# Kernel optimization log

Hardware: AMD Instinct MI355X
Metric: run time of the kernel (lower is better)

Reference implementation:

```python
import jax, jax.numpy as jnp
import numpy as np

B, C, IMG, P, G = 512, 3, 128, 16, 8
DIM, HEADS, DH, DEPTH, MLP, NCLS, K = 384, 6, 64, 12, 1536, 1000, 16
N = G * G + 1  # 65 tokens (cls + 8x8 patches)
INNER = HEADS * DH
PD = C * P * P  # patch_dim = 768


def _rel_pos_index(g):
    coords = np.stack(np.meshgrid(np.arange(g), np.arange(g), indexing='ij')).reshape(2, -1)
    rel = (coords[:, :, None] - coords[:, None, :]).transpose(1, 2, 0)
    rel[..., 0] += g - 1
    rel[..., 1] += g - 1
    rel[..., 0] *= 2 * g - 1
    return jnp.asarray(rel.sum(-1))  # [g*g, g*g] int

REL_IDX = _rel_pos_index(G)


def _ln(x, w, b, eps=1e-5):
    mu = jnp.mean(x, -1, keepdims=True)
    var = jnp.mean((x - mu) ** 2, -1, keepdims=True)
    return (x - mu) * jax.lax.rsqrt(var + eps) * w + b


def setup_inputs() -> dict:
    key = jax.random.key(0)
    ks = iter(jax.random.split(key, 48))
    nrm = lambda shape, s=0.02: jax.random.normal(next(ks), shape, jnp.float32) * s
    return {
        'img': jax.random.normal(next(ks), (B, C, IMG, IMG), jnp.float32),
        'pe_ln1_w': jnp.ones((PD,), jnp.float32), 'pe_ln1_b': jnp.zeros((PD,), jnp.float32),
        'pe_w': nrm((PD, DIM)), 'pe_b': jnp.zeros((DIM,), jnp.float32),
        'pe_ln2_w': jnp.ones((DIM,), jnp.float32), 'pe_ln2_b': jnp.zeros((DIM,), jnp.float32),
        'cls_token': nrm((1, DIM), 1.0), 'pos_emb': nrm((N, DIM), 1.0),
        'attn_ln_w': jnp.ones((DEPTH, DIM), jnp.float32), 'attn_ln_b': jnp.zeros((DEPTH, DIM), jnp.float32),
        'qkv_w': nrm((DEPTH, DIM, 3 * INNER)),
        'out_w': nrm((DEPTH, INNER, DIM)), 'out_b': jnp.zeros((DEPTH, DIM), jnp.float32),
        'bias_tables': nrm((DEPTH, (2 * G - 1) * (2 * G - 1))),
        'ff_ln_w': jnp.ones((DEPTH, DIM), jnp.float32), 'ff_ln_b': jnp.zeros((DEPTH, DIM), jnp.float32),
        'ff_w1': nrm((DEPTH, DIM, MLP)), 'ff_b1': jnp.zeros((DEPTH, MLP), jnp.float32),
        'ff_w2': nrm((DEPTH, MLP, DIM)), 'ff_b2': jnp.zeros((DEPTH, DIM), jnp.float32),
        'final_ln_w': jnp.ones((DIM,), jnp.float32), 'final_ln_b': jnp.zeros((DIM,), jnp.float32),
        'head_w': nrm((DIM, NCLS)), 'head_b': jnp.zeros((NCLS,), jnp.float32),
    }


def reference(img, pe_ln1_w, pe_ln1_b, pe_w, pe_b, pe_ln2_w, pe_ln2_b, cls_token, pos_emb,
              attn_ln_w, attn_ln_b, qkv_w, out_w, out_b, bias_tables,
              ff_ln_w, ff_ln_b, ff_w1, ff_b1, ff_w2, ff_b2,
              final_ln_w, final_ln_b, head_w, head_b):
    b = img.shape[0]
    gh = IMG // P
    # b c (h p1) (w p2) -> b (h w) (p1 p2 c)
    x = img.reshape(b, C, gh, P, gh, P).transpose(0, 2, 4, 3, 5, 1).reshape(b, gh * gh, P * P * C)
    x = _ln(x, pe_ln1_w, pe_ln1_b)
    x = _ln(x @ pe_w + pe_b, pe_ln2_w, pe_ln2_b)
    cls = jnp.broadcast_to(cls_token[None], (b, 1, DIM))
    x = jnp.concatenate([cls, x], axis=1) + pos_emb[:N]
    scale = DH ** -0.5
    neg = jnp.finfo(jnp.float32).min  # == -finfo.max, matching torch masked_fill
    for i in range(DEPTH):
        h = _ln(x, attn_ln_w[i], attn_ln_b[i])
        qkv = h @ qkv_w[i]  # [b, N, 3*INNER]
        q, k, v = jnp.split(qkv, 3, axis=-1)
        q, k, v = [t.reshape(b, N, HEADS, DH).transpose(0, 2, 1, 3) for t in (q, k, v)]
        dots = jnp.einsum('bhid,bhjd->bhij', q, k) * scale
        full_bias = jnp.zeros((N, N), jnp.float32).at[1:, 1:].set(bias_tables[i][REL_IDX])
        dots = dots + full_bias
        _, idx = jax.lax.top_k(dots, K)  # per-query top-k keys
        mask = jnp.put_along_axis(jnp.zeros(dots.shape, bool), idx, True, axis=-1, inplace=False)
        attn = jax.nn.softmax(jnp.where(mask, dots, neg), axis=-1)
        o = jnp.einsum('bhij,bhjd->bhid', attn, v).transpose(0, 2, 1, 3).reshape(b, N, INNER)
        x = o @ out_w[i] + out_b[i] + x
        h = _ln(x, ff_ln_w[i], ff_ln_b[i])
        h = jax.nn.gelu(h @ ff_w1[i] + ff_b1[i], approximate=False)
        x = h @ ff_w2[i] + ff_b2[i] + x
    x = _ln(x, final_ln_w, final_ln_b)
    return x[:, 0] @ head_w + head_b
```

## Files before the change

kernel.cpp:

```cpp
#include <hip/hip_runtime.h>
#include <cstdint>
#include <cstddef>


typedef __attribute__((ext_vector_type(8))) short bf16x8;
typedef __attribute__((ext_vector_type(4))) float f32x4;
typedef __attribute__((ext_vector_type(4))) unsigned short u16x4;

__device__ __forceinline__ unsigned short f2bf(float f) {
  unsigned u = __float_as_uint(f);
  u += 0x7FFF + ((u >> 16) & 1);
  return (unsigned short)(u >> 16);
}
__device__ __forceinline__ float bf2f(unsigned short h) {
  return __uint_as_float(((unsigned)h) << 16);
}
__device__ __forceinline__ float gelu_f(float v) {
  return 0.5f * v * (1.f + erff(v * 0.70710678118654752440f));
}

typedef const __attribute__((address_space(1))) unsigned int* gas1_t;
typedef __attribute__((address_space(3))) unsigned int* las3_t;
__device__ __forceinline__ void async16(const void* g, void* l) {
  __builtin_amdgcn_global_load_lds((gas1_t)g, (las3_t)l, 16, 0, 0);
}

__global__ void k_tconv(const float* __restrict__ in, unsigned short* __restrict__ out,
                        int K, int N, int Npad, int total) {
  int idx = blockIdx.x * 256 + threadIdx.x;
  if (idx >= total) return;
  int per = Npad * K;
  int mat = idx / per;
  int rem = idx - mat * per;
  int n = rem / K;
  int kk = rem - n * K;
  float v = 0.f;
  if (n < N) v = in[(size_t)mat * K * N + (size_t)kk * N + n];
  out[idx] = f2bf(v);
}

__global__ void k_padhb(const float* __restrict__ hb, float* __restrict__ out) {
  int i = blockIdx.x * 256 + threadIdx.x;
  if (i < 1024) out[i] = (i < 1000) ? hb[i] : 0.f;
}

__global__ void k_patchln(const float* __restrict__ img,
                          const float* __restrict__ w1, const float* __restrict__ b1,
                          unsigned short* __restrict__ Xp) {
  const int p = blockIdx.x;
  const int b = p >> 6, pl = p & 63;
  const int gr = pl >> 3, gc = pl & 7;
  const int t = threadIdx.x;
  __shared__ float buf[768];
  __shared__ float ps[4], ps2[4];
#pragma unroll
  for (int s = 0; s < 3; ++s) {
    int rr = s * 16 + (t >> 4);
    int c = rr >> 4, p1 = rr & 15, p2 = t & 15;
    float v = img[(((size_t)b * 3 + c) * 128 + (gr * 16 + p1)) * 128 + gc * 16 + p2];
    buf[(p1 * 16 + p2) * 3 + c] = v;
  }
  __syncthreads();
  float e0 = buf[t], e1 = buf[t + 256], e2 = buf[t + 512];
  float s = e0 + e1 + e2;
  float s2 = e0 * e0 + e1 * e1 + e2 * e2;
  for (int off = 32; off; off >>= 1) { s += __shfl_xor(s, off); s2 += __shfl_xor(s2, off); }
  if ((t & 63) == 0) { ps[t >> 6] = s; ps2[t >> 6] = s2; }
  __syncthreads();
  float S = ps[0] + ps[1] + ps[2] + ps[3];
  float S2 = ps2[0] + ps2[1] + ps2[2] + ps2[3];
  float mu = S * (1.f / 768.f);
  float rs = rsqrtf(S2 * (1.f / 768.f) - mu * mu + 1e-5f);
  size_t ob = (size_t)p * 768;
  Xp[ob + t]       = f2bf((e0 - mu) * rs * w1[t]       + b1[t]);
  Xp[ob + t + 256] = f2bf((e1 - mu) * rs * w1[t + 256] + b1[t + 256]);
  Xp[ob + t + 512] = f2bf((e2 - mu) * rs * w1[t + 512] + b1[t + 512]);
}

__global__ void k_ln384(const float* __restrict__ X, const float* __restrict__ w,
                        const float* __restrict__ bb, unsigned short* __restrict__ H) {
  const int row = blockIdx.x;
  const int t = threadIdx.x;
  const float* xr = X + (size_t)row * 384;
  float e0 = xr[t], e1 = xr[t + 128], e2 = xr[t + 256];
  float s = e0 + e1 + e2, s2 = e0 * e0 + e1 * e1 + e2 * e2;
  for (int off = 32; off; off >>= 1) { s += __shfl_xor(s, off); s2 += __shfl_xor(s2, off); }
  __shared__ float ps[2], ps2[2];
  if ((t & 63) == 0) { ps[t >> 6] = s; ps2[t >> 6] = s2; }
  __syncthreads();
  float S = ps[0] + ps[1], S2 = ps2[0] + ps2[1];
  float mu = S * (1.f / 384.f);
  float rs = rsqrtf(S2 * (1.f / 384.f) - mu * mu + 1e-5f);
  size_t ob = (size_t)row * 384;
  H[ob + t]       = f2bf((e0 - mu) * rs * w[t]       + bb[t]);
  H[ob + t + 128] = f2bf((e1 - mu) * rs * w[t + 128] + bb[t + 128]);
  H[ob + t + 256] = f2bf((e2 - mu) * rs * w[t + 256] + bb[t + 256]);
}

__global__ void k_lncls(const float* __restrict__ X, const float* __restrict__ w,
                        const float* __restrict__ bb, unsigned short* __restrict__ H) {
  const int b = blockIdx.x;
  const int t = threadIdx.x;
  const float* xr = X + (size_t)b * 65 * 384;
  float e0 = xr[t], e1 = xr[t + 128], e2 = xr[t + 256];
  float s = e0 + e1 + e2, s2 = e0 * e0 + e1 * e1 + e2 * e2;
  for (int off = 32; off; off >>= 1) { s += __shfl_xor(s, off); s2 += __shfl_xor(s2, off); }
  __shared__ float ps[2], ps2[2];
  if ((t & 63) == 0) { ps[t >> 6] = s; ps2[t >> 6] = s2; }
  __syncthreads();
  float S = ps[0] + ps[1], S2 = ps2[0] + ps2[1];
  float mu = S * (1.f / 384.f);
  float rs = rsqrtf(S2 * (1.f / 384.f) - mu * mu + 1e-5f);
  size_t ob = (size_t)b * 384;
  H[ob + t]       = f2bf((e0 - mu) * rs * w[t]       + bb[t]);
  H[ob + t + 128] = f2bf((e1 - mu) * rs * w[t + 128] + bb[t + 128]);
  H[ob + t + 256] = f2bf((e2 - mu) * rs * w[t + 256] + bb[t + 256]);
}

__global__ void k_ln2pos(const float* __restrict__ tmp, const float* __restrict__ w,
                         const float* __restrict__ bb, const float* __restrict__ pos,
                         float* __restrict__ Xout) {
  const int p = blockIdx.x;
  const int b = p >> 6, pl = p & 63;
  const int t = threadIdx.x;
  const float* xr = tmp + (size_t)p * 384;
  float e0 = xr[t], e1 = xr[t + 128], e2 = xr[t + 256];
  float s = e0 + e1 + e2, s2 = e0 * e0 + e1 * e1 + e2 * e2;
  for (int off = 32; off; off >>= 1) { s += __shfl_xor(s, off); s2 += __shfl_xor(s2, off); }
  __shared__ float ps[2], ps2[2];
  if ((t & 63) == 0) { ps[t >> 6] = s; ps2[t >> 6] = s2; }
  __syncthreads();
  float S = ps[0] + ps[1], S2 = ps2[0] + ps2[1];
  float mu = S * (1.f / 384.f);
  float rs = rsqrtf(S2 * (1.f / 384.f) - mu * mu + 1e-5f);
  const float* pr = pos + (size_t)(1 + pl) * 384;
  float* orow = Xout + ((size_t)b * 65 + 1 + pl) * 384;
  orow[t]       = (e0 - mu) * rs * w[t]       + bb[t]       + pr[t];
  orow[t + 128] = (e1 - mu) * rs * w[t + 128] + bb[t + 128] + pr[t + 128];
  orow[t + 256] = (e2 - mu) * rs * w[t + 256] + bb[t + 256] + pr[t + 256];
}

__global__ void k_cls(const float* __restrict__ cls, const float* __restrict__ pos,
                      float* __restrict__ Xout) {
  int idx = blockIdx.x * 256 + threadIdx.x;
  if (idx >= 512 * 384) return;
  int b = idx / 384, d = idx - b * 384;
  Xout[(size_t)b * 65 * 384 + d] = cls[d] + pos[d];
}

template <int EPI, int OUTBF>
__global__ __launch_bounds__(256, 2) void k_gemm(
    const unsigned short* __restrict__ A,
    const unsigned short* __restrict__ Wt,
    const float* __restrict__ bias,
    const float* __restrict__ Res,
    void* __restrict__ Out,
    int K, int Nreal) {
  __shared__ alignas(16) unsigned short As[128 * 64];
  __shared__ alignas(16) unsigned short Bs[128 * 64];
  const int t = threadIdx.x;
  const int w = t >> 6, l = t & 63;
  const int m0 = blockIdx.x * 128, n0 = blockIdx.y * 128;
  const int wm = w & 1, wn = w >> 1;

  f32x4 acc[4][4] = {};

  const int rA = t >> 3;
  const int cb = t & 7;
  const unsigned short* Ag = A + (size_t)(m0 + rA) * K + cb * 8;
  const unsigned short* Bg = Wt + (size_t)(n0 + rA) * K + cb * 8;

  for (int k0 = 0; k0 < K; k0 += 64) {
#pragma unroll
    for (int p = 0; p < 4; ++p) {
      async16(Ag + (size_t)(p * 32) * K + k0, &As[p * 2048 + t * 8]);
      async16(Bg + (size_t)(p * 32) * K + k0, &Bs[p * 2048 + t * 8]);
    }
    __syncthreads();
#pragma unroll
    for (int kk = 0; kk < 64; kk += 32) {
      bf16x8 af[4], bfr[4];
      const int kof = kk + (l >> 4) * 8;
      const int rsel = l & 15;
#pragma unroll
      for (int i = 0; i < 4; ++i) {
        af[i]  = *(const bf16x8*)&As[(wm * 64 + i * 16 + rsel) * 64 + kof];
        bfr[i] = *(const bf16x8*)&Bs[(wn * 64 + i * 16 + rsel) * 64 + kof];
      }
#pragma unroll
      for (int i = 0; i < 4; ++i)
#pragma unroll
        for (int j = 0; j < 4; ++j)
          acc[i][j] = __builtin_amdgcn_mfma_f32_16x16x32_bf16(af[i], bfr[j], acc[i][j], 0, 0, 0);
    }
    __syncthreads();
  }

  const int colq = l & 15, rowq = (l >> 4) * 4;
#pragma unroll
  for (int i = 0; i < 4; ++i) {
    const int rb = m0 + wm * 64 + i * 16 + rowq;
#pragma unroll
    for (int j = 0; j < 4; ++j) {
      const int c = n0 + wn * 64 + j * 16 + colq;
      float bv = 0.f;
      if (EPI >= 1) bv = bias[c];
#pragma unroll
      for (int rg = 0; rg < 4; ++rg) {
        const int r = rb + rg;
        float v = acc[i][j][rg] + bv;
        if (EPI == 2) v = gelu_f(v);
        if (EPI == 3) v += Res[(size_t)r * Nreal + c];
        if (c < Nreal) {
          if (OUTBF) ((unsigned short*)Out)[(size_t)r * Nreal + c] = f2bf(v);
          else       ((float*)Out)[(size_t)r * Nreal + c] = v;
        }
      }
    }
  }
}

__global__ __launch_bounds__(256, 4) void k_attn(
    const unsigned short* __restrict__ qkvb,
    const float* __restrict__ btab,
    unsigned short* __restrict__ Obuf) {
  const int blk = blockIdx.x;
  const int b = blk / 6, h = blk - b * 6;
  __shared__ alignas(16) union UU {
    unsigned short qk[2 * 80 * 64];
    float ds[65 * 67];
  } u;
  __shared__ alignas(16) unsigned short vsb[65 * 64];
  __shared__ float wsel[65 * 16];
  __shared__ short seli[65 * 16];
  __shared__ float btl[225];
  const int t = threadIdx.x;
  const size_t base = (size_t)b * 65 * 1152 + h * 64;

  if (t < 225) btl[t] = btab[t];
  for (int idx = t; idx < 520; idx += 256) {
    int r = idx >> 3, c = idx & 7;
    const unsigned short* gp = qkvb + base + (size_t)r * 1152 + c * 8;
    async16(gp, &u.qk[idx * 8]);
    async16(gp + 384, &u.qk[80 * 64 + idx * 8]);
    async16(gp + 768, &vsb[idx * 8]);
  }
  __syncthreads();

  const int w = t >> 6, l = t & 63;
  f32x4 accs[7];
#pragma unroll
  for (int s = 0; s < 7; ++s) {
    int tt = w + s * 4;
    f32x4 a = {0.f, 0.f, 0.f, 0.f};
    if (tt < 25) {
      int it = tt / 5, jt = tt - it * 5;
#pragma unroll
      for (int kk = 0; kk < 64; kk += 32) {
        int kof = kk + (l >> 4) * 8;
        bf16x8 qa = *(const bf16x8*)&u.qk[(it * 16 + (l & 15)) * 64 + kof];
        bf16x8 kb = *(const bf16x8*)&u.qk[80 * 64 + (jt * 16 + (l & 15)) * 64 + kof];
        a = __builtin_amdgcn_mfma_f32_16x16x32_bf16(qa, kb, a, 0, 0, 0);
      }
    }
    accs[s] = a;
  }
  __syncthreads();

#pragma unroll
  for (int s = 0; s < 7; ++s) {
    int tt = w + s * 4;
    if (tt < 25) {
      int it = tt / 5, jt = tt - it * 5;
      int j = jt * 16 + (l & 15);
      int ib = it * 16 + (l >> 4) * 4;
      if (j < 65) {
#pragma unroll
        for (int rg = 0; rg < 4; ++rg) {
          int i = ib + rg;
          if (i < 65) {
            float bias = 0.f;
            if (i > 0 && j > 0) {
              int ri = (i - 1) >> 3, ci = (i - 1) & 7;
              int rj = (j - 1) >> 3, cj = (j - 1) & 7;
              bias = btl[(ri - rj + 7) * 15 + (ci - cj + 7)];
            }
            u.ds[i * 67 + j] = accs[s][rg] * 0.125f + bias;
          }
        }
      }
    }
  }
  __syncthreads();

  if (t < 65) {
    const float* dr = &u.ds[t * 67];
    float lv[16];
#pragma unroll
    for (int i = 0; i < 16; ++i) lv[i] = -3.4e38f;
    for (int j = 0; j < 65; ++j) {
      float x = dr[j];
#pragma unroll
      for (int i = 0; i < 16; ++i) {
        float lo = fminf(lv[i], x);
        lv[i] = fmaxf(lv[i], x);
        x = lo;
      }
    }
    float m0 = lv[0];
    float sum = 0.f;
#pragma unroll
    for (int i = 0; i < 16; ++i) sum += __expf(lv[i] - m0);
    float inv = 1.f / sum;
    float vt = lv[15];
    int pos = 0;
    for (int j = 0; j < 65; ++j) {
      float v = dr[j];
      if (v > vt) {
        wsel[t * 16 + pos] = v;
        seli[t * 16 + pos] = (short)j;
        ++pos;
      }
    }
    for (int j = 0; j < 65; ++j) {
      if (pos >= 16) break;
      float v = dr[j];
      if (v == vt) {
        wsel[t * 16 + pos] = v;
        seli[t * 16 + pos] = (short)j;
        ++pos;
      }
    }
#pragma unroll
    for (int i = 0; i < 16; ++i)
      wsel[t * 16 + i] = __expf(wsel[t * 16 + i] - m0) * inv;
  }
  __syncthreads();

  const size_t obase = (size_t)b * 65 * 384 + h * 64;
  for (int task = t; task < 65 * 16; task += 256) {
    int i = task >> 4, dc = task & 15;
    float a0 = 0.f, a1 = 0.f, a2 = 0.f, a3 = 0.f;
#pragma unroll
    for (int s = 0; s < 16; ++s) {
      float wv = wsel[i * 16 + s];
      int j = seli[i * 16 + s];
      u16x4 raw = *(const u16x4*)&vsb[j * 64 + dc * 4];
      a0 += wv * bf2f(raw.x);
      a1 += wv * bf2f(raw.y);
      a2 += wv * bf2f(raw.z);
      a3 += wv * bf2f(raw.w);
    }
    u16x4 o = {f2bf(a0), f2bf(a1), f2bf(a2), f2bf(a3)};
    *(u16x4*)&Obuf[obase + (size_t)i * 384 + dc * 4] = o;
  }
}

extern "C" void kernel_launch(void* const* d_in, const int* in_sizes, int n_in,
                              void* d_out, int out_size, void* d_ws, size_t ws_size,
                              hipStream_t stream) {
  (void)in_sizes; (void)n_in; (void)out_size; (void)ws_size;
  const float* img       = (const float*)d_in[0];
  const float* pe_ln1_w  = (const float*)d_in[1];
  const float* pe_ln1_b  = (const float*)d_in[2];
  const float* pe_w      = (const float*)d_in[3];
  const float* pe_b      = (const float*)d_in[4];
  const float* pe_ln2_w  = (const float*)d_in[5];
  const float* pe_ln2_b  = (const float*)d_in[6];
  const float* cls_tok   = (const float*)d_in[7];
  const float* pos_emb   = (const float*)d_in[8];
  const float* attn_ln_w = (const float*)d_in[9];
  const float* attn_ln_b = (const float*)d_in[10];
  const float* qkv_w     = (const float*)d_in[11];
  const float* out_w     = (const float*)d_in[12];
  const float* out_b     = (const float*)d_in[13];
  const float* btab      = (const float*)d_in[14];
  const float* ff_ln_w   = (const float*)d_in[15];
  const float* ff_ln_b   = (const float*)d_in[16];
  const float* ff_w1     = (const float*)d_in[17];
  const float* ff_b1     = (const float*)d_in[18];
  const float* ff_w2     = (const float*)d_in[19];
  const float* ff_b2     = (const float*)d_in[20];
  const float* fin_ln_w  = (const float*)d_in[21];
  const float* fin_ln_b  = (const float*)d_in[22];
  const float* head_w    = (const float*)d_in[23];
  const float* head_b    = (const float*)d_in[24];

  char* ws = (char*)d_ws;
  unsigned short* wt_pe   = (unsigned short*)(ws + 0);
  unsigned short* wt_qkv  = (unsigned short*)(ws + 589824);
  unsigned short* wt_out  = (unsigned short*)(ws + 11206656);
  unsigned short* wt_ff1  = (unsigned short*)(ws + 14745600);
  unsigned short* wt_ff2  = (unsigned short*)(ws + 28901376);
  unsigned short* wt_head = (unsigned short*)(ws + 43057152);
  float*          hb_pad  = (float*)(ws + 43843584);
  float*          x       = (float*)(ws + 43847680);
  unsigned short* hbuf    = (unsigned short*)(ws + 94965760);
  unsigned short* qkvb    = (unsigned short*)(ws + 120524800);
  unsigned short* h1      = (unsigned short*)(ws + 197201920);
  unsigned short* xcls    = (unsigned short*)(ws + 299438080);

  unsigned short* Xp = qkvb;
  float* tmp = (float*)h1;

  k_tconv<<<dim3((294912 + 255) / 256), 256, 0, stream>>>(pe_w, wt_pe, 768, 384, 384, 294912);
  k_tconv<<<dim3((5308416 + 255) / 256), 256, 0, stream>>>(qkv_w, wt_qkv, 384, 1152, 1152, 5308416);
  k_tconv<<<dim3((1769472 + 255) / 256), 256, 0, stream>>>(out_w, wt_out, 384, 384, 384, 1769472);
  k_tconv<<<dim3((7077888 + 255) / 256), 256, 0, stream>>>(ff_w1, wt_ff1, 384, 1536, 1536, 7077888);
  k_tconv<<<dim3((7077888 + 255) / 256), 256, 0, stream>>>(ff_w2, wt_ff2, 1536, 384, 384, 7077888);
  k_tconv<<<dim3((393216 + 255) / 256), 256, 0, stream>>>(head_w, wt_head, 384, 1000, 1024, 393216);
  k_padhb<<<4, 256, 0, stream>>>(head_b, hb_pad);

  k_patchln<<<32768, 256, 0, stream>>>(img, pe_ln1_w, pe_ln1_b, Xp);
  k_gemm<1, 0><<<dim3(256, 3), 256, 0, stream>>>(Xp, wt_pe, pe_b, nullptr, tmp, 768, 384);
  k_ln2pos<<<32768, 128, 0, stream>>>(tmp, pe_ln2_w, pe_ln2_b, pos_emb, x);
  k_cls<<<768, 256, 0, stream>>>(cls_tok, pos_emb, x);

  for (int lay = 0; lay < 12; ++lay) {
    k_ln384<<<33280, 128, 0, stream>>>(x, attn_ln_w + lay * 384, attn_ln_b + lay * 384, hbuf);
    k_gemm<0, 1><<<dim3(260, 9), 256, 0, stream>>>(hbuf, wt_qkv + (size_t)lay * 442368,
                                                   nullptr, nullptr, qkvb, 384, 1152);
    k_attn<<<3072, 256, 0, stream>>>(qkvb, btab + lay * 225, hbuf);
    k_gemm<3, 0><<<dim3(260, 3), 256, 0, stream>>>(hbuf, wt_out + (size_t)lay * 147456,
                                                   out_b + lay * 384, x, x, 384, 384);
    k_ln384<<<33280, 128, 0, stream>>>(x, ff_ln_w + lay * 384, ff_ln_b + lay * 384, hbuf);
    k_gemm<2, 1><<<dim3(260, 12), 256, 0, stream>>>(hbuf, wt_ff1 + (size_t)lay * 589824,
                                                    ff_b1 + lay * 1536, nullptr, h1, 384, 1536);
    k_gemm<3, 0><<<dim3(260, 3), 256, 0, stream>>>(h1, wt_ff2 + (size_t)lay * 589824,
                                                   ff_b2 + lay * 384, x, x, 1536, 384);
  }

  k_lncls<<<512, 128, 0, stream>>>(x, fin_ln_w, fin_ln_b, xcls);
  k_gemm<1, 0><<<dim3(4, 8), 256, 0, stream>>>(xcls, wt_head, hb_pad, nullptr, d_out, 384, 1000);
}
```

Baseline: 5.523 ms.

## Split attention into score kernel and top-k/softmax/PV kernel with transposed scores

The fused attention kernel is split in two. The first computes Q·K^T plus bias and writes a transposed fp32 score matrix to global scratch. The second reloads the scores and V, then runs the serial top-k selection spread across 65 of 128 threads in two wavefronts with conflict-free column reads, followed by the PV accumulation. The aim is to stop the single-wavefront top-k step from stalling a large block and to raise occupancy, at the cost of an extra global round-trip of about 4420 floats per (batch, head) and one more launch per layer.

```diff
diff --git a/kernel.cpp b/kernel.cpp
--- a/kernel.cpp
+++ b/kernel.cpp
@@ -220,19 +220,16 @@
   }
 }
 
-__global__ __launch_bounds__(256, 4) void k_attn(
+__global__ __launch_bounds__(256, 4) void k_attnA(
     const unsigned short* __restrict__ qkvb,
     const float* __restrict__ btab,
-    unsigned short* __restrict__ Obuf) {
+    float* __restrict__ scores) {
   const int blk = blockIdx.x;
   const int b = blk / 6, h = blk - b * 6;
   __shared__ alignas(16) union UU {
     unsigned short qk[2 * 80 * 64];
-    float ds[65 * 67];
+    float ds[65 * 68];
   } u;
-  __shared__ alignas(16) unsigned short vsb[65 * 64];
-  __shared__ float wsel[65 * 16];
-  __shared__ short seli[65 * 16];
   __shared__ float btl[225];
   const int t = threadIdx.x;
   const size_t base = (size_t)b * 65 * 1152 + h * 64;
@@ -243,7 +240,6 @@
     const unsigned short* gp = qkvb + base + (size_t)r * 1152 + c * 8;
     async16(gp, &u.qk[idx * 8]);
     async16(gp + 384, &u.qk[80 * 64 + idx * 8]);
-    async16(gp + 768, &vsb[idx * 8]);
   }
   __syncthreads();
 
@@ -254,13 +250,13 @@
     int tt = w + s * 4;
     f32x4 a = {0.f, 0.f, 0.f, 0.f};
     if (tt < 25) {
-      int it = tt / 5, jt = tt - it * 5;
+      int ti = tt / 5, tq = tt - ti * 5;
 #pragma unroll
       for (int kk = 0; kk < 64; kk += 32) {
         int kof = kk + (l >> 4) * 8;
-        bf16x8 qa = *(const bf16x8*)&u.qk[(it * 16 + (l & 15)) * 64 + kof];
-        bf16x8 kb = *(const bf16x8*)&u.qk[80 * 64 + (jt * 16 + (l & 15)) * 64 + kof];
-        a = __builtin_amdgcn_mfma_f32_16x16x32_bf16(qa, kb, a, 0, 0, 0);
+        bf16x8 kb = *(const bf16x8*)&u.qk[80 * 64 + (ti * 16 + (l & 15)) * 64 + kof];
+        bf16x8 qa = *(const bf16x8*)&u.qk[(tq * 16 + (l & 15)) * 64 + kof];
+        a = __builtin_amdgcn_mfma_f32_16x16x32_bf16(kb, qa, a, 0, 0, 0);
       }
     }
     accs[s] = a;
@@ -271,21 +267,21 @@
   for (int s = 0; s < 7; ++s) {
     int tt = w + s * 4;
     if (tt < 25) {
-      int it = tt / 5, jt = tt - it * 5;
-      int j = jt * 16 + (l & 15);
-      int ib = it * 16 + (l >> 4) * 4;
-      if (j < 65) {
+      int ti = tt / 5, tq = tt - ti * 5;
+      int i = tq * 16 + (l & 15);
+      int jb = ti * 16 + (l >> 4) * 4;
+      if (i < 65) {
 #pragma unroll
         for (int rg = 0; rg < 4; ++rg) {
-          int i = ib + rg;
-          if (i < 65) {
+          int j = jb + rg;
+          if (j < 65) {
             float bias = 0.f;
             if (i > 0 && j > 0) {
               int ri = (i - 1) >> 3, ci = (i - 1) & 7;
               int rj = (j - 1) >> 3, cj = (j - 1) & 7;
               bias = btl[(ri - rj + 7) * 15 + (ci - cj + 7)];
             }
-            u.ds[i * 67 + j] = accs[s][rg] * 0.125f + bias;
+            u.ds[j * 68 + i] = accs[s][rg] * 0.125f + bias;
           }
         }
       }
@@ -293,13 +289,43 @@
   }
   __syncthreads();
 
-  if (t < 65) {
-    const float* dr = &u.ds[t * 67];
+  float* sg = scores + (size_t)blk * 4420;
+  for (int idx = t; idx < 1105; idx += 256)
+    *(f32x4*)(sg + idx * 4) = *(const f32x4*)&u.ds[idx * 4];
+}
+
+__global__ __launch_bounds__(128, 2) void k_attnB(
+    const unsigned short* __restrict__ qkvb,
+    const float* __restrict__ scores,
+    unsigned short* __restrict__ Obuf) {
+  const int blk = blockIdx.x;
+  const int b = blk / 6, h = blk - b * 6;
+  __shared__ alignas(16) float scl[65 * 68];
+  __shared__ alignas(16) unsigned short vsb[65 * 72];
+  __shared__ float wsel[65 * 16];
+  __shared__ short seli[65 * 16];
+  const int t = threadIdx.x;
+  const size_t base = (size_t)b * 65 * 1152 + h * 64;
+  const float* sg = scores + (size_t)blk * 4420;
+
+  for (int idx = t; idx < 1105; idx += 128)
+    async16(sg + idx * 4, &scl[idx * 4]);
+  for (int idx = t; idx < 520; idx += 128) {
+    int r = idx >> 3, c = idx & 7;
+    bf16x8 raw = *(const bf16x8*)(qkvb + base + (size_t)r * 1152 + 768 + c * 8);
+    *(bf16x8*)&vsb[r * 72 + c * 8] = raw;
+  }
+  __syncthreads();
+
+  const int wv = t >> 6, l = t & 63;
+  const int r = 2 * l + wv;
+  const bool act = wv ? (l < 32) : (l <= 32);
+  if (act) {
     float lv[16];
 #pragma unroll
     for (int i = 0; i < 16; ++i) lv[i] = -3.4e38f;
     for (int j = 0; j < 65; ++j) {
-      float x = dr[j];
+      float x = scl[j * 68 + r];
 #pragma unroll
       for (int i = 0; i < 16; ++i) {
         float lo = fminf(lv[i], x);
@@ -315,41 +341,37 @@
     float vt = lv[15];
     int pos = 0;
     for (int j = 0; j < 65; ++j) {
-      float v = dr[j];
-      if (v > vt) {
-        wsel[t * 16 + pos] = v;
-        seli[t * 16 + pos] = (short)j;
+      float v = scl[j * 68 + r];
+      if (v > vt && pos < 16) {
+        wsel[r * 16 + pos] = __expf(v - m0) * inv;
+        seli[r * 16 + pos] = (short)j;
         ++pos;
       }
     }
     for (int j = 0; j < 65; ++j) {
-      if (pos >= 16) break;
-      float v = dr[j];
-      if (v == vt) {
-        wsel[t * 16 + pos] = v;
-        seli[t * 16 + pos] = (short)j;
+      float v = scl[j * 68 + r];
+      if (v == vt && pos < 16) {
+        wsel[r * 16 + pos] = __expf(v - m0) * inv;
+        seli[r * 16 + pos] = (short)j;
         ++pos;
       }
     }
-#pragma unroll
-    for (int i = 0; i < 16; ++i)
-      wsel[t * 16 + i] = __expf(wsel[t * 16 + i] - m0) * inv;
   }
   __syncthreads();
 
   const size_t obase = (size_t)b * 65 * 384 + h * 64;
-  for (int task = t; task < 65 * 16; task += 256) {
+  for (int task = t; task < 65 * 16; task += 128) {
     int i = task >> 4, dc = task & 15;
     float a0 = 0.f, a1 = 0.f, a2 = 0.f, a3 = 0.f;
 #pragma unroll
     for (int s = 0; s < 16; ++s) {
-      float wv = wsel[i * 16 + s];
+      float wv2 = wsel[i * 16 + s];
       int j = seli[i * 16 + s];
-      u16x4 raw = *(const u16x4*)&vsb[j * 64 + dc * 4];
-      a0 += wv * bf2f(raw.x);
-      a1 += wv * bf2f(raw.y);
-      a2 += wv * bf2f(raw.z);
-      a3 += wv * bf2f(raw.w);
+      u16x4 raw = *(const u16x4*)&vsb[j * 72 + dc * 4];
+      a0 += wv2 * bf2f(raw.x);
+      a1 += wv2 * bf2f(raw.y);
+      a2 += wv2 * bf2f(raw.z);
+      a3 += wv2 * bf2f(raw.w);
     }
     u16x4 o = {f2bf(a0), f2bf(a1), f2bf(a2), f2bf(a3)};
     *(u16x4*)&Obuf[obase + (size_t)i * 384 + dc * 4] = o;
@@ -402,6 +424,7 @@
 
   unsigned short* Xp = qkvb;
   float* tmp = (float*)h1;
+  float* scoresb = (float*)h1;
 
   k_tconv<<<dim3((294912 + 255) / 256), 256, 0, stream>>>(pe_w, wt_pe, 768, 384, 384, 294912);
   k_tconv<<<dim3((5308416 + 255) / 256), 256, 0, stream>>>(qkv_w, wt_qkv, 384, 1152, 1152, 5308416);
@@ -420,7 +443,8 @@
     k_ln384<<<33280, 128, 0, stream>>>(x, attn_ln_w + lay * 384, attn_ln_b + lay * 384, hbuf);
     k_gemm<0, 1><<<dim3(260, 9), 256, 0, stream>>>(hbuf, wt_qkv + (size_t)lay * 442368,
                                                    nullptr, nullptr, qkvb, 384, 1152);
-    k_attn<<<3072, 256, 0, stream>>>(qkvb, btab + lay * 225, hbuf);
+    k_attnA<<<3072, 256, 0, stream>>>(qkvb, btab + lay * 225, scoresb);
+    k_attnB<<<3072, 128, 0, stream>>>(qkvb, scoresb, hbuf);
     k_gemm<3, 0><<<dim3(260, 3), 256, 0, stream>>>(hbuf, wt_out + (size_t)lay * 147456,
                                                    out_b + lay * 384, x, x, 384, 384);
     k_ln384<<<33280, 128, 0, stream>>>(x, ff_ln_w + lay * 384, ff_ln_b + lay * 384, hbuf);
```

New measurement: 5.692 ms. +3.1%, slower.

## Split attention into score, top-k and weighted-V kernels with packed sort keys

Applied to the files above, without the earlier changes.

The single attention kernel, where only 65 of 256 threads ran the serial top-k, is split into three kernels. The first writes scaled, biased scores to global memory. The second uses one thread per query row across the whole grid to select the top 16 with packed float-and-index keys and two interleaved sorted lists, then writes weight/index pairs. The third gathers V with those pairs. This spreads the top-k work over all lanes, at the cost of extra global round trips for scores and pairs, two more launches, and 7 low mantissa bits of each score truncated in the comparison keys, which can change tie-breaking.

```diff
diff --git a/kernel.cpp b/kernel.cpp
--- a/kernel.cpp
+++ b/kernel.cpp
@@ -220,19 +220,16 @@
   }
 }
 
-__global__ __launch_bounds__(256, 4) void k_attn(
+__global__ __launch_bounds__(256, 4) void k_attnA(
     const unsigned short* __restrict__ qkvb,
     const float* __restrict__ btab,
-    unsigned short* __restrict__ Obuf) {
+    float* __restrict__ scores) {
   const int blk = blockIdx.x;
   const int b = blk / 6, h = blk - b * 6;
   __shared__ alignas(16) union UU {
     unsigned short qk[2 * 80 * 64];
-    float ds[65 * 67];
+    float ds[65 * 68];
   } u;
-  __shared__ alignas(16) unsigned short vsb[65 * 64];
-  __shared__ float wsel[65 * 16];
-  __shared__ short seli[65 * 16];
   __shared__ float btl[225];
   const int t = threadIdx.x;
   const size_t base = (size_t)b * 65 * 1152 + h * 64;
@@ -243,7 +240,6 @@
     const unsigned short* gp = qkvb + base + (size_t)r * 1152 + c * 8;
     async16(gp, &u.qk[idx * 8]);
     async16(gp + 384, &u.qk[80 * 64 + idx * 8]);
-    async16(gp + 768, &vsb[idx * 8]);
   }
   __syncthreads();
 
@@ -285,7 +281,7 @@
               int rj = (j - 1) >> 3, cj = (j - 1) & 7;
               bias = btl[(ri - rj + 7) * 15 + (ci - cj + 7)];
             }
-            u.ds[i * 67 + j] = accs[s][rg] * 0.125f + bias;
+            u.ds[i * 68 + j] = accs[s][rg] * 0.125f + bias;
           }
         }
       }
@@ -293,59 +289,105 @@
   }
   __syncthreads();
 
-  if (t < 65) {
-    const float* dr = &u.ds[t * 67];
-    float lv[16];
-#pragma unroll
-    for (int i = 0; i < 16; ++i) lv[i] = -3.4e38f;
-    for (int j = 0; j < 65; ++j) {
-      float x = dr[j];
-#pragma unroll
-      for (int i = 0; i < 16; ++i) {
-        float lo = fminf(lv[i], x);
-        lv[i] = fmaxf(lv[i], x);
-        x = lo;
-      }
-    }
-    float m0 = lv[0];
-    float sum = 0.f;
-#pragma unroll
-    for (int i = 0; i < 16; ++i) sum += __expf(lv[i] - m0);
-    float inv = 1.f / sum;
-    float vt = lv[15];
-    int pos = 0;
-    for (int j = 0; j < 65; ++j) {
-      float v = dr[j];
-      if (v > vt) {
-        wsel[t * 16 + pos] = v;
-        seli[t * 16 + pos] = (short)j;
-        ++pos;
-      }
-    }
-    for (int j = 0; j < 65; ++j) {
-      if (pos >= 16) break;
-      float v = dr[j];
-      if (v == vt) {
-        wsel[t * 16 + pos] = v;
-        seli[t * 16 + pos] = (short)j;
-        ++pos;
-      }
-    }
-#pragma unroll
-    for (int i = 0; i < 16; ++i)
-      wsel[t * 16 + i] = __expf(wsel[t * 16 + i] - m0) * inv;
+  float* sg = scores + (size_t)blk * 4420;
+  for (int idx = t; idx < 1105; idx += 256)
+    *(f32x4*)(sg + idx * 4) = *(const f32x4*)&u.ds[idx * 4];
+}
+
+__device__ __forceinline__ unsigned mkkey(float v, int j) {
+  unsigned bits = __float_as_uint(v);
+  unsigned m = (unsigned)(((int)bits) >> 31) | 0x80000000u;
+  return ((bits ^ m) & 0xFFFFFF80u) | (unsigned)(127 - j);
+}
+__device__ __forceinline__ float deckey(unsigned k) {
+  unsigned kb = k & 0xFFFFFF80u;
+  unsigned bb = (kb & 0x80000000u) ? (kb ^ 0x80000000u) : ~kb;
+  return __uint_as_float(bb);
+}
+__device__ __forceinline__ void cas16(unsigned* lv, unsigned x) {
+#pragma unroll
+  for (int i = 0; i < 16; ++i) {
+    unsigned lo = min(lv[i], x);
+    lv[i] = max(lv[i], x);
+    x = lo;
+  }
+}
+
+__global__ __launch_bounds__(256) void k_attnT(
+    const float* __restrict__ scores,
+    float* __restrict__ pairs) {
+  const int R = blockIdx.x * 256 + threadIdx.x;
+  const int blk = R / 65, i = R - blk * 65;
+  const float* row = scores + (size_t)blk * 4420 + (size_t)i * 68;
+
+  unsigned lvA[16], lvB[16];
+#pragma unroll
+  for (int s = 0; s < 16; ++s) { lvA[s] = 0u; lvB[s] = 0u; }
+
+#pragma unroll
+  for (int c = 0; c < 16; ++c) {
+    f32x4 v4 = *(const f32x4*)(row + c * 4);
+    int j0 = c * 4;
+    unsigned k0 = mkkey(v4.x, j0);
+    unsigned k1 = mkkey(v4.y, j0 + 1);
+    unsigned k2 = mkkey(v4.z, j0 + 2);
+    unsigned k3 = mkkey(v4.w, j0 + 3);
+    cas16(lvA, k0); cas16(lvB, k1); cas16(lvA, k2); cas16(lvB, k3);
+  }
+  cas16(lvA, mkkey(row[64], 64));
+
+  unsigned C[16];
+#pragma unroll
+  for (int s = 0; s < 16; ++s) C[s] = max(lvA[s], lvB[15 - s]);
+
+  float m0 = deckey(max(lvA[0], lvB[0]));
+  float e[16];
+  float sum = 0.f;
+#pragma unroll
+  for (int s = 0; s < 16; ++s) { e[s] = __expf(deckey(C[s]) - m0); sum += e[s]; }
+  float inv = 1.f / sum;
+
+  float out[32];
+#pragma unroll
+  for (int s = 0; s < 16; ++s) {
+    out[2 * s] = e[s] * inv;
+    out[2 * s + 1] = __int_as_float(127 - (int)(C[s] & 0x7Fu));
+  }
+  float* og = pairs + (size_t)R * 32;
+#pragma unroll
+  for (int s = 0; s < 8; ++s)
+    *(f32x4*)(og + s * 4) = *(const f32x4*)&out[s * 4];
+}
+
+__global__ __launch_bounds__(128, 4) void k_attnV(
+    const unsigned short* __restrict__ qkvb,
+    const float* __restrict__ pairs,
+    unsigned short* __restrict__ Obuf) {
+  const int blk = blockIdx.x;
+  const int b = blk / 6, h = blk - b * 6;
+  __shared__ alignas(16) unsigned short vsb[65 * 72];
+  __shared__ alignas(16) float prs[65 * 32];
+  const int t = threadIdx.x;
+  const size_t base = (size_t)b * 65 * 1152 + h * 64;
+  const float* pg = pairs + (size_t)blk * 65 * 32;
+
+  for (int idx = t; idx < 520; idx += 128) {
+    int r = idx >> 3, c = idx & 7;
+    bf16x8 raw = *(const bf16x8*)(qkvb + base + (size_t)r * 1152 + 768 + c * 8);
+    *(bf16x8*)&vsb[r * 72 + c * 8] = raw;
+    *(f32x4*)&prs[idx * 4] = *(const f32x4*)(pg + idx * 4);
   }
   __syncthreads();
 
   const size_t obase = (size_t)b * 65 * 384 + h * 64;
-  for (int task = t; task < 65 * 16; task += 256) {
+  for (int task = t; task < 65 * 16; task += 128) {
     int i = task >> 4, dc = task & 15;
     float a0 = 0.f, a1 = 0.f, a2 = 0.f, a3 = 0.f;
 #pragma unroll
     for (int s = 0; s < 16; ++s) {
-      float wv = wsel[i * 16 + s];
-      int j = seli[i * 16 + s];
-      u16x4 raw = *(const u16x4*)&vsb[j * 64 + dc * 4];
+      float wv = prs[i * 32 + 2 * s];
+      int j = __float_as_int(prs[i * 32 + 2 * s + 1]);
+      u16x4 raw = *(const u16x4*)&vsb[j * 72 + dc * 4];
       a0 += wv * bf2f(raw.x);
       a1 += wv * bf2f(raw.y);
       a2 += wv * bf2f(raw.z);
@@ -402,6 +444,8 @@
 
   unsigned short* Xp = qkvb;
   float* tmp = (float*)h1;
+  float* scoresb = (float*)h1;
+  float* pairsb  = (float*)(ws + 251514880);
 
   k_tconv<<<dim3((294912 + 255) / 256), 256, 0, stream>>>(pe_w, wt_pe, 768, 384, 384, 294912);
   k_tconv<<<dim3((5308416 + 255) / 256), 256, 0, stream>>>(qkv_w, wt_qkv, 384, 1152, 1152, 5308416);
@@ -420,7 +464,9 @@
     k_ln384<<<33280, 128, 0, stream>>>(x, attn_ln_w + lay * 384, attn_ln_b + lay * 384, hbuf);
     k_gemm<0, 1><<<dim3(260, 9), 256, 0, stream>>>(hbuf, wt_qkv + (size_t)lay * 442368,
                                                    nullptr, nullptr, qkvb, 384, 1152);
-    k_attn<<<3072, 256, 0, stream>>>(qkvb, btab + lay * 225, hbuf);
+    k_attnA<<<3072, 256, 0, stream>>>(qkvb, btab + lay * 225, scoresb);
+    k_attnT<<<780, 256, 0, stream>>>(scoresb, pairsb);
+    k_attnV<<<3072, 128, 0, stream>>>(qkvb, pairsb, hbuf);
     k_gemm<3, 0><<<dim3(260, 3), 256, 0, stream>>>(hbuf, wt_out + (size_t)lay * 147456,
                                                    out_b + lay * 384, x, x, 384, 384);
     k_ln384<<<33280, 128, 0, stream>>>(x, ff_ln_w + lay * 384, ff_ln_b + lay * 384, hbuf);
```

Result: faster. 5.071 ms (-8.2%).
